# Kernel tuning notes

Hardware: AMD Instinct MI355X
Metric: run time of the kernel (lower is better)

Reference implementation:

```python
import jax, jax.numpy as jnp
import numpy as np

N_NODES = 100000
N_EDGES = 400000
N_GRAPHS = 2500
DIM = 128
F_IN = 78
N_LAYERS = 3
BN_EPS = 1e-5


def setup_inputs() -> dict:
    key = jax.random.key(0)
    ks = jax.random.split(key, 24)
    def lin(k, fi, fo):
        return jax.random.normal(k, (fi, fo), jnp.float32) / np.sqrt(fi)
    inp = {
        "x": jax.random.normal(ks[0], (N_NODES, F_IN), jnp.float32),
        "edge_index": jax.random.randint(ks[1], (2, N_EDGES), 0, N_NODES, jnp.int32),
        "batch": jnp.sort(jax.random.randint(ks[2], (N_NODES,), 0, N_GRAPHS, jnp.int32)),
        "num_graphs": N_GRAPHS,
        "gcn1_W": lin(ks[3], F_IN, DIM), "gcn1_b": jnp.zeros((DIM,), jnp.float32),
        "gcn2_W": lin(ks[4], DIM, DIM), "gcn2_b": jnp.zeros((DIM,), jnp.float32),
        "gin0_w1": lin(ks[5], F_IN, DIM), "gin0_b1": jnp.zeros((DIM,), jnp.float32),
        "gin0_w2": lin(ks[6], DIM, DIM), "gin0_b2": jnp.zeros((DIM,), jnp.float32),
        # layers 1..2 stacked (same 128->128 shapes)
        "gin_w1": jnp.stack([lin(ks[7], DIM, DIM), lin(ks[8], DIM, DIM)]),
        "gin_b1": jnp.zeros((2, DIM), jnp.float32),
        "gin_w2": jnp.stack([lin(ks[9], DIM, DIM), lin(ks[10], DIM, DIM)]),
        "gin_b2": jnp.zeros((2, DIM), jnp.float32),
        "bn_gamma": jnp.ones((N_LAYERS, DIM), jnp.float32),
        "bn_beta": jnp.zeros((N_LAYERS, DIM), jnp.float32),
    }
    return inp


def reference(x, edge_index, batch, num_graphs,
              gcn1_W, gcn1_b, gcn2_W, gcn2_b,
              gin0_w1, gin0_b1, gin0_w2, gin0_b2,
              gin_w1, gin_b1, gin_w2, gin_b2,
              bn_gamma, bn_beta):
    n = x.shape[0]
    src, dst = edge_index[0], edge_index[1]

    def gcn(h, W, b):
        # linear -> symmetric-normalized aggregation with self loops (PyG GCNConv)
        h = h @ W
        loop = jnp.arange(n, dtype=src.dtype)
        s = jnp.concatenate([src, loop])
        d = jnp.concatenate([dst, loop])
        deg = jax.ops.segment_sum(jnp.ones(s.shape[0], h.dtype), d, num_segments=n)
        dis = jax.lax.rsqrt(deg)  # deg >= 1 thanks to self loops
        norm = (dis[s] * dis[d])[:, None]
        return jax.ops.segment_sum(h[s] * norm, d, num_segments=n) + b

    def gin(h, w1, b1, w2, b2):
        # GINConv, eps=0: mlp(x + sum_{j->i} x_j)
        agg = jax.ops.segment_sum(h[src], dst, num_segments=n)
        z = jax.nn.relu((h + agg) @ w1 + b1)
        return z @ w2 + b2

    def bn(h, g, bt):
        mu = h.mean(0)
        var = ((h - mu) ** 2).mean(0)
        return (h - mu) * jax.lax.rsqrt(var + BN_EPS) * g + bt

    g1 = jax.nn.relu(gcn(x, gcn1_W, gcn1_b))
    g2 = jax.nn.relu(gcn(g1, gcn2_W, gcn2_b))
    g2a = g2 + g1
    g2m = g2 * g1

    h = x
    xs = []
    m = jnp.float32(1.0)
    e = jnp.float32(0.0)
    for i in range(N_LAYERS):
        if i == 0:
            h = gin(h, gin0_w1, gin0_b1, gin0_w2, gin0_b2)
        else:
            h = gin(h, gin_w1[i - 1], gin_b1[i - 1], gin_w2[i - 1], gin_b2[i - 1])
        h = bn(jax.nn.relu(h), bn_gamma[i], bn_beta[i])
        m = m * h
        e = e + h
        xs.append(h)

    rep = jnp.concatenate(xs + [m, e, g1, g2, g2a, g2m], axis=-1)  # [N, 9*DIM]
    return jax.ops.segment_max(rep, batch, num_segments=num_graphs)
```

## Files before the change

kernel.cpp:

```cpp
#include <hip/hip_runtime.h>
#include <math.h>

#define DIMC 128
#define FINC 78
#define REPW 1152
#define SCAN_TILE 1024

typedef __attribute__((ext_vector_type(8))) short short8x;
typedef __attribute__((ext_vector_type(4))) float f32x4;

__device__ inline float b2f(unsigned short u) {
    union { unsigned int i; float f; } v; v.i = ((unsigned int)u) << 16; return v.f;
}
__device__ inline unsigned short f2b(float f) {
    union { float f; unsigned int i; } v; v.f = f;
    unsigned int r = (v.i + 0x7FFFu + ((v.i >> 16) & 1u)) >> 16;
    return (unsigned short)r;
}


__global__ void k_fill_int(int* __restrict__ p, int v, int n) {
    int i = blockIdx.x * blockDim.x + threadIdx.x;
    if (i < n) p[i] = v;
}

__global__ void k_fill(float* __restrict__ p, float v, int n) {
    int i = blockIdx.x * blockDim.x + threadIdx.x;
    if (i < n) p[i] = v;
}

__global__ void k_count(const int* __restrict__ dst, int* __restrict__ cnt, int E) {
    int e = blockIdx.x * blockDim.x + threadIdx.x;
    if (e < E) atomicAdd(&cnt[dst[e]], 1);
}

__launch_bounds__(256)
__global__ void k_tilesum(const int* __restrict__ cnt, int* __restrict__ tileSum, int N) {
    __shared__ int red[256];
    int base = blockIdx.x * SCAN_TILE;
    int s = 0;
    for (int i = threadIdx.x; i < SCAN_TILE; i += 256) {
        int idx = base + i;
        if (idx < N) s += cnt[idx];
    }
    red[threadIdx.x] = s;
    __syncthreads();
    for (int d = 128; d > 0; d >>= 1) {
        if (threadIdx.x < d) red[threadIdx.x] += red[threadIdx.x + d];
        __syncthreads();
    }
    if (threadIdx.x == 0) tileSum[blockIdx.x] = red[0];
}

__launch_bounds__(256)
__global__ void k_tilescan(const int* __restrict__ tileSum, int* __restrict__ tileOff,
                           int* __restrict__ rowptr, int T, int N) {
    __shared__ int sh[256];
    int t = threadIdx.x;
    int orig = (t < T) ? tileSum[t] : 0;
    sh[t] = orig;
    __syncthreads();
    for (int d = 1; d < 256; d <<= 1) {
        int v = (t >= d) ? sh[t - d] : 0;
        __syncthreads();
        sh[t] += v;
        __syncthreads();
    }
    if (t < T) tileOff[t] = sh[t] - orig;
    if (t == 255) rowptr[N] = sh[255];
}

__launch_bounds__(256)
__global__ void k_tileemit(const int* __restrict__ cnt, const int* __restrict__ tileOff,
                           int* __restrict__ rowptr, int* __restrict__ cursor,
                           float* __restrict__ dis, int N) {
    __shared__ int sh[256];
    int t = threadIdx.x;
    int base = blockIdx.x * SCAN_TILE;
    int idx0 = base + t * 4;
    int v0 = 0, v1 = 0, v2 = 0, v3 = 0;
    if (idx0 + 3 < N) {
        int4 v = *(const int4*)(cnt + idx0);
        v0 = v.x; v1 = v.y; v2 = v.z; v3 = v.w;
    } else {
        if (idx0 + 0 < N) v0 = cnt[idx0 + 0];
        if (idx0 + 1 < N) v1 = cnt[idx0 + 1];
        if (idx0 + 2 < N) v2 = cnt[idx0 + 2];
        if (idx0 + 3 < N) v3 = cnt[idx0 + 3];
    }
    int s0 = v0, s1 = s0 + v1, s2 = s1 + v2, s3 = s2 + v3;
    sh[t] = s3;
    __syncthreads();
    for (int d = 1; d < 256; d <<= 1) {
        int v = (t >= d) ? sh[t - d] : 0;
        __syncthreads();
        sh[t] += v;
        __syncthreads();
    }
    int gbase = tileOff[blockIdx.x] + ((t == 0) ? 0 : sh[t - 1]);
    int ex[4] = {0, s0, s1, s2};
    int vv[4] = {v0, v1, v2, v3};
#pragma unroll
    for (int j = 0; j < 4; ++j) {
        int idx = idx0 + j;
        if (idx < N) {
            int r = gbase + ex[j];
            rowptr[idx] = r;
            cursor[idx] = r;
            dis[idx] = rsqrtf((float)vv[j] + 1.0f);
        }
    }
}

__global__ void k_scatter(const int* __restrict__ src, const int* __restrict__ dst,
                          int* __restrict__ cursor, int* __restrict__ col, int E) {
    int e = blockIdx.x * blockDim.x + threadIdx.x;
    if (e < E) {
        int pos = atomicAdd(&cursor[dst[e]], 1);
        col[pos] = src[e];
    }
}

__global__ void k_bounds(const int* __restrict__ batch, int* __restrict__ start, int N, int G) {
    int g = blockIdx.x * blockDim.x + threadIdx.x;
    if (g <= G) {
        int lo = 0, hi = N;
        while (lo < hi) { int mid = (lo + hi) >> 1; if (batch[mid] < g) lo = mid + 1; else hi = mid; }
        start[g] = lo;
    }
}


__global__ void k_cvt_w(const float* __restrict__ s0, const float* __restrict__ s1,
                        const float* __restrict__ s2, const float* __restrict__ s3,
                        const float* __restrict__ s4, const float* __restrict__ s5,
                        const float* __restrict__ s6, const float* __restrict__ s7,
                        unsigned short* __restrict__ whi, unsigned short* __restrict__ wlo) {
    int my = blockIdx.y;
    const float* src; int Ksrc, KP; size_t dstoff;
    const size_t o96 = (size_t)128 * 96, o128 = (size_t)128 * 128;
    switch (my) {
        case 0: src = s0; Ksrc = 78;  KP = 96;  dstoff = 0; break;
        case 1: src = s1; Ksrc = 78;  KP = 96;  dstoff = o96; break;
        case 2: src = s2; Ksrc = 128; KP = 128; dstoff = 2 * o96; break;
        case 3: src = s3; Ksrc = 128; KP = 128; dstoff = 2 * o96 + o128; break;
        case 4: src = s4; Ksrc = 128; KP = 128; dstoff = 2 * o96 + 2 * o128; break;
        case 5: src = s5; Ksrc = 128; KP = 128; dstoff = 2 * o96 + 3 * o128; break;
        case 6: src = s6; Ksrc = 128; KP = 128; dstoff = 2 * o96 + 4 * o128; break;
        default: src = s7; Ksrc = 128; KP = 128; dstoff = 2 * o96 + 5 * o128; break;
    }
    int i = blockIdx.x * blockDim.x + threadIdx.x;
    if (i < 128 * KP) {
        int n = i / KP, k = i - n * KP;
        float v = (k < Ksrc) ? src[(size_t)k * DIMC + n] : 0.f;
        unsigned short hi = f2b(v);
        unsigned short lo = f2b(v - b2f(hi));
        whi[dstoff + i] = hi;
        wlo[dstoff + i] = lo;
    }
}


template<int KREAL, int KP>
__launch_bounds__(256)
__global__ void k_gemm_mfma3(const float* __restrict__ A,
                             const unsigned short* __restrict__ Whi,
                             const unsigned short* __restrict__ Wlo,
                             const float* __restrict__ bias,
                             const float* __restrict__ rowScale,
                             const float* __restrict__ inScale,
                             const float* __restrict__ inShift,
                             float* __restrict__ statsOut,
                             float* __restrict__ C, int N, int doRelu) {
    __shared__ unsigned short sAhi[128 * 32];
    __shared__ unsigned short sAlo[128 * 32];
    __shared__ unsigned short sBhi[128 * 32];
    __shared__ unsigned short sBlo[128 * 32];
    __shared__ float sStats[256];
    const int tid = threadIdx.x;
    const int row0 = blockIdx.x * 128;

    const int wave = tid >> 6;
    const int lane = tid & 63;
    const int lm = lane & 15, q = lane >> 4;
    const int wr = (wave >> 1) * 64, wc = (wave & 1) * 64;

    f32x4 acc[4][4];
#pragma unroll
    for (int a = 0; a < 4; ++a)
#pragma unroll
        for (int b = 0; b < 4; ++b) acc[a][b] = (f32x4){0.f, 0.f, 0.f, 0.f};

    for (int k0 = 0; k0 < KP; k0 += 32) {
        if (k0) __syncthreads();
        for (int s = tid; s < 512; s += 256) {
            int r = s >> 2, g = s & 3;
            int gr = row0 + r;
            float v[8];
            int kb = k0 + g * 8;
            if (gr < N) {
                if (KREAL % 8 == 0) {
                    float4 u0 = *(const float4*)(A + (size_t)gr * KREAL + kb);
                    float4 u1 = *(const float4*)(A + (size_t)gr * KREAL + kb + 4);
                    v[0] = u0.x; v[1] = u0.y; v[2] = u0.z; v[3] = u0.w;
                    v[4] = u1.x; v[5] = u1.y; v[6] = u1.z; v[7] = u1.w;
                } else {
#pragma unroll
                    for (int j = 0; j < 8; ++j) {
                        int k = kb + j;
                        v[j] = (k < KREAL) ? A[(size_t)gr * KREAL + k] : 0.f;
                    }
                }
                if (inScale) {
#pragma unroll
                    for (int j = 0; j < 8; ++j) {
                        int k = kb + j;
                        v[j] = fmaf(v[j], inScale[k], inShift[k]);
                    }
                }
            } else {
#pragma unroll
                for (int j = 0; j < 8; ++j) v[j] = 0.f;
            }
            unsigned int hi[4], lo[4];
#pragma unroll
            for (int j = 0; j < 4; ++j) {
                unsigned short h0 = f2b(v[2 * j]), h1 = f2b(v[2 * j + 1]);
                unsigned short l0 = f2b(v[2 * j] - b2f(h0)), l1 = f2b(v[2 * j + 1] - b2f(h1));
                hi[j] = (unsigned int)h0 | ((unsigned int)h1 << 16);
                lo[j] = (unsigned int)l0 | ((unsigned int)l1 << 16);
            }
            size_t addr = ((size_t)g * 128 + ((r + g) & 127)) * 8;
            *(uint4*)(sAhi + addr) = make_uint4(hi[0], hi[1], hi[2], hi[3]);
            *(uint4*)(sAlo + addr) = make_uint4(lo[0], lo[1], lo[2], lo[3]);
        }
        for (int s = tid; s < 512; s += 256) {
            int n = s >> 2, g = s & 3;
            size_t gaddr = (size_t)n * KP + k0 + g * 8;
            size_t addr = ((size_t)g * 128 + ((n + g) & 127)) * 8;
            *(uint4*)(sBhi + addr) = *(const uint4*)(Whi + gaddr);
            *(uint4*)(sBlo + addr) = *(const uint4*)(Wlo + gaddr);
        }
        __syncthreads();

        short8x ah[4], al[4], bh[4], bl[4];
#pragma unroll
        for (int rt = 0; rt < 4; ++rt) {
            int m = wr + rt * 16 + lm;
            size_t addr = ((size_t)q * 128 + ((m + q) & 127)) * 8;
            ah[rt] = *(const short8x*)(sAhi + addr);
            al[rt] = *(const short8x*)(sAlo + addr);
        }
#pragma unroll
        for (int ct = 0; ct < 4; ++ct) {
            int n = wc + ct * 16 + lm;
            size_t addr = ((size_t)q * 128 + ((n + q) & 127)) * 8;
            bh[ct] = *(const short8x*)(sBhi + addr);
            bl[ct] = *(const short8x*)(sBlo + addr);
        }
#pragma unroll
        for (int rt = 0; rt < 4; ++rt)
#pragma unroll
            for (int ct = 0; ct < 4; ++ct) {
                acc[rt][ct] = __builtin_amdgcn_mfma_f32_16x16x32_bf16(ah[rt], bh[ct], acc[rt][ct], 0, 0, 0);
                acc[rt][ct] = __builtin_amdgcn_mfma_f32_16x16x32_bf16(ah[rt], bl[ct], acc[rt][ct], 0, 0, 0);
                acc[rt][ct] = __builtin_amdgcn_mfma_f32_16x16x32_bf16(al[rt], bh[ct], acc[rt][ct], 0, 0, 0);
            }
    }

    float cs[4] = {0.f, 0.f, 0.f, 0.f}, cq[4] = {0.f, 0.f, 0.f, 0.f};
#pragma unroll
    for (int rt = 0; rt < 4; ++rt) {
#pragma unroll
        for (int i = 0; i < 4; ++i) {
            int row = wr + rt * 16 + q * 4 + i;
            int gr = row0 + row;
            if (gr < N) {
                float sc = rowScale ? rowScale[gr] : 1.f;
#pragma unroll
                for (int ct = 0; ct < 4; ++ct) {
                    int colg = wc + ct * 16 + lm;
                    float v = acc[rt][ct][i];
                    if (bias) v += bias[colg];
                    if (doRelu) v = fmaxf(v, 0.f);
                    v *= sc;
                    C[(size_t)gr * DIMC + colg] = v;
                    if (statsOut) { cs[ct] += v; cq[ct] = fmaf(v, v, cq[ct]); }
                }
            }
        }
    }
    if (statsOut) {
        sStats[tid] = 0.f;
        __syncthreads();
#pragma unroll
        for (int ct = 0; ct < 4; ++ct) {
            int colg = wc + ct * 16 + lm;
            atomicAdd(&sStats[colg], cs[ct]);
            atomicAdd(&sStats[128 + colg], cq[ct]);
        }
        __syncthreads();
        atomicAdd(&statsOut[tid], sStats[tid]);
    }
}


__global__ void k_bn_coef(const float* __restrict__ bnsum, const float* __restrict__ gamma,
                          const float* __restrict__ beta, float* __restrict__ coef, float invN) {
    int c = threadIdx.x;
    float mu  = bnsum[c] * invN;
    float var = bnsum[128 + c] * invN - mu * mu;
    float inv = rsqrtf(var + 1e-5f);
    float s = gamma[c] * inv;
    coef[c] = s;
    coef[128 + c] = beta[c] - mu * s;
}


__global__ void k_gather_gcn(const float4* __restrict__ t, const int* __restrict__ rowptr,
                             const int* __restrict__ col, const float* __restrict__ dis,
                             const float4* __restrict__ bias, float4* __restrict__ out, int N) {
    int i = blockIdx.x * blockDim.x + threadIdx.x;
    int node = i >> 5, c4 = i & 31;
    if (node >= N) return;
    int s = rowptr[node], e = rowptr[node + 1];
    float4 acc = t[(size_t)node * 32 + c4];
    for (int k = s; k < e; ++k) {
        float4 v = t[(size_t)col[k] * 32 + c4];
        acc.x += v.x; acc.y += v.y; acc.z += v.z; acc.w += v.w;
    }
    float d = dis[node];
    float4 b = bias[c4];
    float4 o;
    o.x = fmaxf(acc.x * d + b.x, 0.f);
    o.y = fmaxf(acc.y * d + b.y, 0.f);
    o.z = fmaxf(acc.z * d + b.z, 0.f);
    o.w = fmaxf(acc.w * d + b.w, 0.f);
    out[(size_t)node * 32 + c4] = o;
}

__global__ void k_gather_gin(const float4* __restrict__ t, const int* __restrict__ rowptr,
                             const int* __restrict__ col, const float4* __restrict__ bias,
                             float4* __restrict__ out, int N) {
    int i = blockIdx.x * blockDim.x + threadIdx.x;
    int node = i >> 5, c4 = i & 31;
    if (node >= N) return;
    int s = rowptr[node], e = rowptr[node + 1];
    float4 acc = t[(size_t)node * 32 + c4];
    for (int k = s; k < e; ++k) {
        float4 v = t[(size_t)col[k] * 32 + c4];
        acc.x += v.x; acc.y += v.y; acc.z += v.z; acc.w += v.w;
    }
    float4 b = bias[c4];
    float4 o;
    o.x = fmaxf(acc.x + b.x, 0.f);
    o.y = fmaxf(acc.y + b.y, 0.f);
    o.z = fmaxf(acc.z + b.z, 0.f);
    o.w = fmaxf(acc.w + b.w, 0.f);
    out[(size_t)node * 32 + c4] = o;
}


__global__ void k_segmax_gin_all(const float* __restrict__ h0, const float* __restrict__ h1,
                                 const float* __restrict__ h2, const float* __restrict__ coef,
                                 const int* __restrict__ start, float* __restrict__ out) {
    int g = blockIdx.x, c = threadIdx.x;
    float s0 = coef[c],       t0 = coef[128 + c];
    float s1 = coef[256 + c], t1 = coef[384 + c];
    float s2 = coef[512 + c], t2 = coef[640 + c];
    int s = start[g], e = start[g + 1];
    float m0 = -INFINITY, m1 = -INFINITY, m2 = -INFINITY, mm = -INFINITY, me = -INFINITY;
    for (int n = s; n < e; ++n) {
        size_t idx = (size_t)n * DIMC + c;
        float a0 = fmaf(h0[idx], s0, t0);
        float a1 = fmaf(h1[idx], s1, t1);
        float a2 = fmaf(h2[idx], s2, t2);
        m0 = fmaxf(m0, a0); m1 = fmaxf(m1, a1); m2 = fmaxf(m2, a2);
        mm = fmaxf(mm, a0 * a1 * a2);
        me = fmaxf(me, a0 + a1 + a2);
    }
    size_t o = (size_t)g * REPW + c;
    out[o]            = m0;
    out[o + 1 * DIMC] = m1;
    out[o + 2 * DIMC] = m2;
    out[o + 3 * DIMC] = mm;
    out[o + 4 * DIMC] = me;
}

__global__ void k_segmax_gcn(const float* __restrict__ G1, const float* __restrict__ G2,
                             const int* __restrict__ start, float* __restrict__ out) {
    int g = blockIdx.x, c = threadIdx.x;
    int s = start[g], e = start[g + 1];
    float m1 = -INFINITY, m2 = -INFINITY, ma = -INFINITY, mm = -INFINITY;
    for (int n = s; n < e; ++n) {
        float a = G1[(size_t)n * DIMC + c], b = G2[(size_t)n * DIMC + c];
        m1 = fmaxf(m1, a); m2 = fmaxf(m2, b);
        ma = fmaxf(ma, a + b); mm = fmaxf(mm, a * b);
    }
    size_t o = (size_t)g * REPW + c;
    out[o + 5 * DIMC] = m1;
    out[o + 6 * DIMC] = m2;
    out[o + 7 * DIMC] = ma;
    out[o + 8 * DIMC] = mm;
}


extern "C" void kernel_launch(void* const* d_in, const int* in_sizes, int n_in,
                              void* d_out, int out_size, void* d_ws, size_t ws_size,
                              hipStream_t stream) {
    const float* x       = (const float*)d_in[0];
    const int*   ei      = (const int*)d_in[1];
    const int*   batch   = (const int*)d_in[2];
    const float* gcn1_W  = (const float*)d_in[4];
    const float* gcn1_b  = (const float*)d_in[5];
    const float* gcn2_W  = (const float*)d_in[6];
    const float* gcn2_b  = (const float*)d_in[7];
    const float* gin0_w1 = (const float*)d_in[8];
    const float* gin0_b1 = (const float*)d_in[9];
    const float* gin0_w2 = (const float*)d_in[10];
    const float* gin0_b2 = (const float*)d_in[11];
    const float* gin_w1  = (const float*)d_in[12];
    const float* gin_b1  = (const float*)d_in[13];
    const float* gin_w2  = (const float*)d_in[14];
    const float* gin_b2  = (const float*)d_in[15];
    const float* bn_g    = (const float*)d_in[16];
    const float* bn_b    = (const float*)d_in[17];
    float* out = (float*)d_out;

    const int N = in_sizes[0] / FINC;
    const int E = in_sizes[1] / 2;
    const int G = out_size / REPW;
    const int* srcv = ei;
    const int* dstv = ei + E;

    char* ws = (char*)d_ws;
    size_t off = 0;
    auto alloc = [&](size_t bytes) { char* p = ws + off; off += (bytes + 255) & ~(size_t)255; return p; };
    int*   cnt     = (int*)alloc(N * 4);
    int*   rowptr  = (int*)alloc((N + 1) * 4);
    int*   cursor  = (int*)alloc(N * 4);
    int*   col     = (int*)alloc(E * 4);
    float* dis     = (float*)alloc(N * 4);
    float* bnsum   = (float*)alloc(768 * 4);
    float* coef    = (float*)alloc(768 * 4);
    int*   start   = (int*)alloc((G + 1) * 4);
    int*   tileSum = (int*)alloc(256 * 4);
    int*   tileOff = (int*)alloc(256 * 4);
    const size_t wtElems = 2 * (size_t)128 * 96 + 6 * (size_t)128 * 128;
    unsigned short* whi = (unsigned short*)alloc(wtElems * 2);
    unsigned short* wlo = (unsigned short*)alloc(wtElems * 2);
    float* bufT    = (float*)alloc((size_t)N * DIMC * 4);
    float* bufZ    = (float*)alloc((size_t)N * DIMC * 4);
    float* h0      = (float*)alloc((size_t)N * DIMC * 4);
    float* h1      = (float*)alloc((size_t)N * DIMC * 4);
    float* h2      = (float*)alloc((size_t)N * DIMC * 4);
    (void)ws_size; (void)n_in;

    const size_t o96 = (size_t)128 * 96, o128 = (size_t)128 * 128;
    const size_t woff[8] = {0, o96, 2 * o96, 2 * o96 + o128, 2 * o96 + 2 * o128,
                            2 * o96 + 3 * o128, 2 * o96 + 4 * o128, 2 * o96 + 5 * o128};

    const int T = 256;
    auto cdiv = [](long a, long b) { return (int)((a + b - 1) / b); };
    const int gemmGrid = cdiv(N, 128);
    const int gatherGrid = cdiv((long)N * 32, T);
    const int nTiles = cdiv(N, SCAN_TILE);
    const float invN = 1.0f / (float)N;

    k_fill_int<<<cdiv(N, T), T, 0, stream>>>(cnt, 0, N);
    k_count<<<cdiv(E, T), T, 0, stream>>>(dstv, cnt, E);
    k_tilesum<<<nTiles, T, 0, stream>>>(cnt, tileSum, N);
    k_tilescan<<<1, T, 0, stream>>>(tileSum, tileOff, rowptr, nTiles, N);
    k_tileemit<<<nTiles, T, 0, stream>>>(cnt, tileOff, rowptr, cursor, dis, N);
    k_scatter<<<cdiv(E, T), T, 0, stream>>>(srcv, dstv, cursor, col, E);
    k_bounds<<<cdiv(G + 1, T), T, 0, stream>>>(batch, start, N, G);
    k_fill<<<3, T, 0, stream>>>(bnsum, 0.f, 768);
    {
        dim3 g(64, 8);
        k_cvt_w<<<g, T, 0, stream>>>(gcn1_W, gin0_w1, gcn2_W, gin0_w2,
                                     gin_w1, gin_w1 + o128, gin_w2, gin_w2 + o128, whi, wlo);
    }

    k_gemm_mfma3<FINC, 96><<<gemmGrid, T, 0, stream>>>(x, whi + woff[0], wlo + woff[0],
                                                       nullptr, dis, nullptr, nullptr, nullptr, bufT, N, 0);
    k_gather_gcn<<<gatherGrid, T, 0, stream>>>((const float4*)bufT, rowptr, col, dis,
                                               (const float4*)gcn1_b, (float4*)bufZ, N);
    k_gemm_mfma3<DIMC, 128><<<gemmGrid, T, 0, stream>>>(bufZ, whi + woff[2], wlo + woff[2],
                                                        nullptr, dis, nullptr, nullptr, nullptr, bufT, N, 0);
    k_gather_gcn<<<gatherGrid, T, 0, stream>>>((const float4*)bufT, rowptr, col, dis,
                                               (const float4*)gcn2_b, (float4*)h0, N);
    k_segmax_gcn<<<G, DIMC, 0, stream>>>(bufZ, h0, start, out);

    const int w1i[3] = {1, 4, 5};
    const int w2i[3] = {3, 6, 7};
    const float* b1s[3] = {gin0_b1, gin_b1, gin_b1 + DIMC};
    const float* b2s[3] = {gin0_b2, gin_b2, gin_b2 + DIMC};
    float* hs[3] = {h0, h1, h2};

    for (int L = 0; L < 3; ++L) {
        if (L == 0)
            k_gemm_mfma3<FINC, 96><<<gemmGrid, T, 0, stream>>>(x, whi + woff[1], wlo + woff[1],
                                                               nullptr, nullptr, nullptr, nullptr, nullptr,
                                                               bufT, N, 0);
        else
            k_gemm_mfma3<DIMC, 128><<<gemmGrid, T, 0, stream>>>(hs[L - 1], whi + woff[w1i[L]], wlo + woff[w1i[L]],
                                                                nullptr, nullptr,
                                                                coef + (L - 1) * 256, coef + (L - 1) * 256 + 128,
                                                                nullptr, bufT, N, 0);
        k_gather_gin<<<gatherGrid, T, 0, stream>>>((const float4*)bufT, rowptr, col,
                                                   (const float4*)b1s[L], (float4*)bufZ, N);
        k_gemm_mfma3<DIMC, 128><<<gemmGrid, T, 0, stream>>>(bufZ, whi + woff[w2i[L]], wlo + woff[w2i[L]],
                                                            b2s[L], nullptr, nullptr, nullptr,
                                                            bnsum + L * 256, hs[L], N, 1);
        k_bn_coef<<<1, DIMC, 0, stream>>>(bnsum + L * 256, bn_g + L * DIMC, bn_b + L * DIMC,
                                          coef + L * 256, invN);
    }

    k_segmax_gin_all<<<G, DIMC, 0, stream>>>(h0, h1, h2, coef, start, out);
}
```

Measured before the change: 794.1 us.

## Store intermediates as split bf16 hi/lo pairs and fold BN into GIN weights

All node-feature intermediates now live as pairs of bf16 hi/lo arrays instead of fp32. The GEMM loads pre-split operands directly rather than converting fp32 on every tile, and the gathers read and write the hi/lo form eight channels per thread. Batch-norm scale is folded into the next layer's W1 and its shift into a per-column bias applied in the gather, which drops the per-element affine transform in the GEMM prologue. Storage footprint is unchanged, but the gathers and epilogues take on extra pack/unpack work.

```diff
diff --git a/kernel.cpp b/kernel.cpp
--- a/kernel.cpp
+++ b/kernel.cpp
@@ -16,6 +16,26 @@
     union { float f; unsigned int i; } v; v.f = f;
     unsigned int r = (v.i + 0x7FFFu + ((v.i >> 16) & 1u)) >> 16;
     return (unsigned short)r;
+}
+__device__ inline void hl2f8(uint4 h, uint4 l, float* f) {
+    unsigned int hw[4] = {h.x, h.y, h.z, h.w}, lw[4] = {l.x, l.y, l.z, l.w};
+#pragma unroll
+    for (int j = 0; j < 4; ++j) {
+        f[2 * j]     = b2f((unsigned short)(hw[j] & 0xFFFF)) + b2f((unsigned short)(lw[j] & 0xFFFF));
+        f[2 * j + 1] = b2f((unsigned short)(hw[j] >> 16))    + b2f((unsigned short)(lw[j] >> 16));
+    }
+}
+__device__ inline void f82hl(const float* f, uint4& h, uint4& l) {
+    unsigned int hw[4], lw[4];
+#pragma unroll
+    for (int j = 0; j < 4; ++j) {
+        unsigned short h0 = f2b(f[2 * j]), h1 = f2b(f[2 * j + 1]);
+        unsigned short l0 = f2b(f[2 * j] - b2f(h0)), l1 = f2b(f[2 * j + 1] - b2f(h1));
+        hw[j] = (unsigned int)h0 | ((unsigned int)h1 << 16);
+        lw[j] = (unsigned int)l0 | ((unsigned int)l1 << 16);
+    }
+    h = make_uint4(hw[0], hw[1], hw[2], hw[3]);
+    l = make_uint4(lw[0], lw[1], lw[2], lw[3]);
 }
 
 
@@ -131,10 +151,21 @@
 }
 
 
+__global__ void k_cvt_x(const float* __restrict__ x, unsigned short* __restrict__ xhi,
+                        unsigned short* __restrict__ xlo, int N) {
+    int i = blockIdx.x * blockDim.x + threadIdx.x;
+    if (i < N * 96) {
+        int n = i / 96, k = i - n * 96;
+        float v = (k < FINC) ? x[(size_t)n * FINC + k] : 0.f;
+        unsigned short hi = f2b(v);
+        xhi[i] = hi;
+        xlo[i] = f2b(v - b2f(hi));
+    }
+}
+
 __global__ void k_cvt_w(const float* __restrict__ s0, const float* __restrict__ s1,
                         const float* __restrict__ s2, const float* __restrict__ s3,
                         const float* __restrict__ s4, const float* __restrict__ s5,
-                        const float* __restrict__ s6, const float* __restrict__ s7,
                         unsigned short* __restrict__ whi, unsigned short* __restrict__ wlo) {
     int my = blockIdx.y;
     const float* src; int Ksrc, KP; size_t dstoff;
@@ -145,165 +176,50 @@
         case 2: src = s2; Ksrc = 128; KP = 128; dstoff = 2 * o96; break;
         case 3: src = s3; Ksrc = 128; KP = 128; dstoff = 2 * o96 + o128; break;
         case 4: src = s4; Ksrc = 128; KP = 128; dstoff = 2 * o96 + 2 * o128; break;
-        case 5: src = s5; Ksrc = 128; KP = 128; dstoff = 2 * o96 + 3 * o128; break;
-        case 6: src = s6; Ksrc = 128; KP = 128; dstoff = 2 * o96 + 4 * o128; break;
-        default: src = s7; Ksrc = 128; KP = 128; dstoff = 2 * o96 + 5 * o128; break;
+        default: src = s5; Ksrc = 128; KP = 128; dstoff = 2 * o96 + 3 * o128; break;
     }
     int i = blockIdx.x * blockDim.x + threadIdx.x;
     if (i < 128 * KP) {
         int n = i / KP, k = i - n * KP;
         float v = (k < Ksrc) ? src[(size_t)k * DIMC + n] : 0.f;
         unsigned short hi = f2b(v);
-        unsigned short lo = f2b(v - b2f(hi));
+        wlo[dstoff + i] = f2b(v - b2f(hi));
         whi[dstoff + i] = hi;
-        wlo[dstoff + i] = lo;
-    }
-}
-
-
-template<int KREAL, int KP>
+    }
+}
+
+
 __launch_bounds__(256)
-__global__ void k_gemm_mfma3(const float* __restrict__ A,
-                             const unsigned short* __restrict__ Whi,
-                             const unsigned short* __restrict__ Wlo,
-                             const float* __restrict__ bias,
-                             const float* __restrict__ rowScale,
-                             const float* __restrict__ inScale,
-                             const float* __restrict__ inShift,
-                             float* __restrict__ statsOut,
-                             float* __restrict__ C, int N, int doRelu) {
-    __shared__ unsigned short sAhi[128 * 32];
-    __shared__ unsigned short sAlo[128 * 32];
-    __shared__ unsigned short sBhi[128 * 32];
-    __shared__ unsigned short sBlo[128 * 32];
-    __shared__ float sStats[256];
-    const int tid = threadIdx.x;
-    const int row0 = blockIdx.x * 128;
-
-    const int wave = tid >> 6;
-    const int lane = tid & 63;
-    const int lm = lane & 15, q = lane >> 4;
-    const int wr = (wave >> 1) * 64, wc = (wave & 1) * 64;
-
-    f32x4 acc[4][4];
-#pragma unroll
-    for (int a = 0; a < 4; ++a)
-#pragma unroll
-        for (int b = 0; b < 4; ++b) acc[a][b] = (f32x4){0.f, 0.f, 0.f, 0.f};
-
-    for (int k0 = 0; k0 < KP; k0 += 32) {
-        if (k0) __syncthreads();
-        for (int s = tid; s < 512; s += 256) {
-            int r = s >> 2, g = s & 3;
-            int gr = row0 + r;
-            float v[8];
-            int kb = k0 + g * 8;
-            if (gr < N) {
-                if (KREAL % 8 == 0) {
-                    float4 u0 = *(const float4*)(A + (size_t)gr * KREAL + kb);
-                    float4 u1 = *(const float4*)(A + (size_t)gr * KREAL + kb + 4);
-                    v[0] = u0.x; v[1] = u0.y; v[2] = u0.z; v[3] = u0.w;
-                    v[4] = u1.x; v[5] = u1.y; v[6] = u1.z; v[7] = u1.w;
-                } else {
-#pragma unroll
-                    for (int j = 0; j < 8; ++j) {
-                        int k = kb + j;
-                        v[j] = (k < KREAL) ? A[(size_t)gr * KREAL + k] : 0.f;
-                    }
-                }
-                if (inScale) {
-#pragma unroll
-                    for (int j = 0; j < 8; ++j) {
-                        int k = kb + j;
-                        v[j] = fmaf(v[j], inScale[k], inShift[k]);
-                    }
-                }
-            } else {
-#pragma unroll
-                for (int j = 0; j < 8; ++j) v[j] = 0.f;
-            }
-            unsigned int hi[4], lo[4];
-#pragma unroll
-            for (int j = 0; j < 4; ++j) {
-                unsigned short h0 = f2b(v[2 * j]), h1 = f2b(v[2 * j + 1]);
-                unsigned short l0 = f2b(v[2 * j] - b2f(h0)), l1 = f2b(v[2 * j + 1] - b2f(h1));
-                hi[j] = (unsigned int)h0 | ((unsigned int)h1 << 16);
-                lo[j] = (unsigned int)l0 | ((unsigned int)l1 << 16);
-            }
-            size_t addr = ((size_t)g * 128 + ((r + g) & 127)) * 8;
-            *(uint4*)(sAhi + addr) = make_uint4(hi[0], hi[1], hi[2], hi[3]);
-            *(uint4*)(sAlo + addr) = make_uint4(lo[0], lo[1], lo[2], lo[3]);
-        }
-        for (int s = tid; s < 512; s += 256) {
-            int n = s >> 2, g = s & 3;
-            size_t gaddr = (size_t)n * KP + k0 + g * 8;
-            size_t addr = ((size_t)g * 128 + ((n + g) & 127)) * 8;
-            *(uint4*)(sBhi + addr) = *(const uint4*)(Whi + gaddr);
-            *(uint4*)(sBlo + addr) = *(const uint4*)(Wlo + gaddr);
-        }
-        __syncthreads();
-
-        short8x ah[4], al[4], bh[4], bl[4];
-#pragma unroll
-        for (int rt = 0; rt < 4; ++rt) {
-            int m = wr + rt * 16 + lm;
-            size_t addr = ((size_t)q * 128 + ((m + q) & 127)) * 8;
-            ah[rt] = *(const short8x*)(sAhi + addr);
-            al[rt] = *(const short8x*)(sAlo + addr);
-        }
-#pragma unroll
-        for (int ct = 0; ct < 4; ++ct) {
-            int n = wc + ct * 16 + lm;
-            size_t addr = ((size_t)q * 128 + ((n + q) & 127)) * 8;
-            bh[ct] = *(const short8x*)(sBhi + addr);
-            bl[ct] = *(const short8x*)(sBlo + addr);
-        }
-#pragma unroll
-        for (int rt = 0; rt < 4; ++rt)
-#pragma unroll
-            for (int ct = 0; ct < 4; ++ct) {
-                acc[rt][ct] = __builtin_amdgcn_mfma_f32_16x16x32_bf16(ah[rt], bh[ct], acc[rt][ct], 0, 0, 0);
-                acc[rt][ct] = __builtin_amdgcn_mfma_f32_16x16x32_bf16(ah[rt], bl[ct], acc[rt][ct], 0, 0, 0);
-                acc[rt][ct] = __builtin_amdgcn_mfma_f32_16x16x32_bf16(al[rt], bh[ct], acc[rt][ct], 0, 0, 0);
-            }
-    }
-
-    float cs[4] = {0.f, 0.f, 0.f, 0.f}, cq[4] = {0.f, 0.f, 0.f, 0.f};
-#pragma unroll
-    for (int rt = 0; rt < 4; ++rt) {
-#pragma unroll
-        for (int i = 0; i < 4; ++i) {
-            int row = wr + rt * 16 + q * 4 + i;
-            int gr = row0 + row;
-            if (gr < N) {
-                float sc = rowScale ? rowScale[gr] : 1.f;
-#pragma unroll
-                for (int ct = 0; ct < 4; ++ct) {
-                    int colg = wc + ct * 16 + lm;
-                    float v = acc[rt][ct][i];
-                    if (bias) v += bias[colg];
-                    if (doRelu) v = fmaxf(v, 0.f);
-                    v *= sc;
-                    C[(size_t)gr * DIMC + colg] = v;
-                    if (statsOut) { cs[ct] += v; cq[ct] = fmaf(v, v, cq[ct]); }
-                }
-            }
-        }
-    }
-    if (statsOut) {
-        sStats[tid] = 0.f;
-        __syncthreads();
-#pragma unroll
-        for (int ct = 0; ct < 4; ++ct) {
-            int colg = wc + ct * 16 + lm;
-            atomicAdd(&sStats[colg], cs[ct]);
-            atomicAdd(&sStats[128 + colg], cq[ct]);
-        }
-        __syncthreads();
-        atomicAdd(&statsOut[tid], sStats[tid]);
-    }
-}
-
+__global__ void k_bn_w(const float* __restrict__ bnsum, const float* __restrict__ gamma,
+                       const float* __restrict__ beta, const float* __restrict__ w1,
+                       float* __restrict__ coef, unsigned short* __restrict__ whiO,
+                       unsigned short* __restrict__ wloO, float* __restrict__ cbeta, float invN) {
+    __shared__ float sS[128], sT[128], sC[256];
+    int t = threadIdx.x;
+    if (t < 128) {
+        float mu  = bnsum[t] * invN;
+        float var = bnsum[128 + t] * invN - mu * mu;
+        float inv = rsqrtf(var + 1e-5f);
+        float s = gamma[t] * inv;
+        float sh = beta[t] - mu * s;
+        coef[t] = s; coef[128 + t] = sh;
+        sS[t] = s; sT[t] = sh;
+    }
+    __syncthreads();
+    for (int i = t; i < 16384; i += 256) {
+        int n = i >> 7, k = i & 127;
+        float v = w1[(size_t)k * 128 + n] * sS[k];
+        unsigned short hi = f2b(v);
+        whiO[i] = hi;
+        wloO[i] = f2b(v - b2f(hi));
+    }
+    int n = t & 127, half = t >> 7;
+    float acc = 0.f;
+    for (int k = half * 64; k < half * 64 + 64; ++k) acc = fmaf(sT[k], w1[(size_t)k * 128 + n], acc);
+    sC[t] = acc;
+    __syncthreads();
+    if (t < 128) cbeta[t] = sC[t] + sC[t + 128];
+}
 
 __global__ void k_bn_coef(const float* __restrict__ bnsum, const float* __restrict__ gamma,
                           const float* __restrict__ beta, float* __restrict__ coef, float invN) {
@@ -317,53 +233,182 @@
 }
 
 
-__global__ void k_gather_gcn(const float4* __restrict__ t, const int* __restrict__ rowptr,
-                             const int* __restrict__ col, const float* __restrict__ dis,
-                             const float4* __restrict__ bias, float4* __restrict__ out, int N) {
+template<int KP>
+__launch_bounds__(256)
+__global__ void k_gemm_hl(const unsigned short* __restrict__ Ahi,
+                          const unsigned short* __restrict__ Alo,
+                          const unsigned short* __restrict__ Whi,
+                          const unsigned short* __restrict__ Wlo,
+                          const float* __restrict__ bias,
+                          const float* __restrict__ rowScale,
+                          float* __restrict__ statsOut,
+                          unsigned short* __restrict__ Chi,
+                          unsigned short* __restrict__ Clo,
+                          int N, int doRelu) {
+    __shared__ unsigned short sAhi[4096], sAlo[4096], sBhi[4096], sBlo[4096];
+    __shared__ float sStats[256];
+    const int tid = threadIdx.x;
+    const int row0 = blockIdx.x * 128;
+
+    const int wave = tid >> 6;
+    const int lane = tid & 63;
+    const int lm = lane & 15, q = lane >> 4;
+    const int wr = (wave >> 1) * 64, wc = (wave & 1) * 64;
+
+    f32x4 acc[4][4];
+#pragma unroll
+    for (int a = 0; a < 4; ++a)
+#pragma unroll
+        for (int b = 0; b < 4; ++b) acc[a][b] = (f32x4){0.f, 0.f, 0.f, 0.f};
+
+    for (int k0 = 0; k0 < KP; k0 += 32) {
+        if (k0) __syncthreads();
+        for (int s = tid; s < 512; s += 256) {
+            int g = s & 3, r = s >> 2;
+            int gr = row0 + r;
+            size_t la = ((size_t)g * 128 + r) * 8;
+            uint4 vh = make_uint4(0, 0, 0, 0), vl = make_uint4(0, 0, 0, 0);
+            if (gr < N) {
+                size_t ga = (size_t)gr * KP + k0 + g * 8;
+                vh = *(const uint4*)(Ahi + ga);
+                vl = *(const uint4*)(Alo + ga);
+            }
+            *(uint4*)(sAhi + la) = vh;
+            *(uint4*)(sAlo + la) = vl;
+            size_t gb = (size_t)r * KP + k0 + g * 8;
+            *(uint4*)(sBhi + la) = *(const uint4*)(Whi + gb);
+            *(uint4*)(sBlo + la) = *(const uint4*)(Wlo + gb);
+        }
+        __syncthreads();
+
+        short8x ah[4], al[4], bh[4], bl[4];
+#pragma unroll
+        for (int rt = 0; rt < 4; ++rt) {
+            size_t addr = ((size_t)q * 128 + wr + rt * 16 + lm) * 8;
+            ah[rt] = *(const short8x*)(sAhi + addr);
+            al[rt] = *(const short8x*)(sAlo + addr);
+        }
+#pragma unroll
+        for (int ct = 0; ct < 4; ++ct) {
+            size_t addr = ((size_t)q * 128 + wc + ct * 16 + lm) * 8;
+            bh[ct] = *(const short8x*)(sBhi + addr);
+            bl[ct] = *(const short8x*)(sBlo + addr);
+        }
+#pragma unroll
+        for (int rt = 0; rt < 4; ++rt)
+#pragma unroll
+            for (int ct = 0; ct < 4; ++ct) {
+                acc[rt][ct] = __builtin_amdgcn_mfma_f32_16x16x32_bf16(ah[rt], bh[ct], acc[rt][ct], 0, 0, 0);
+                acc[rt][ct] = __builtin_amdgcn_mfma_f32_16x16x32_bf16(ah[rt], bl[ct], acc[rt][ct], 0, 0, 0);
+                acc[rt][ct] = __builtin_amdgcn_mfma_f32_16x16x32_bf16(al[rt], bh[ct], acc[rt][ct], 0, 0, 0);
+            }
+    }
+
+    float cs[4] = {0.f, 0.f, 0.f, 0.f}, cq[4] = {0.f, 0.f, 0.f, 0.f};
+#pragma unroll
+    for (int rt = 0; rt < 4; ++rt) {
+#pragma unroll
+        for (int i = 0; i < 4; ++i) {
+            int row = wr + rt * 16 + q * 4 + i;
+            int gr = row0 + row;
+            if (gr < N) {
+                float sc = rowScale ? rowScale[gr] : 1.f;
+#pragma unroll
+                for (int ct = 0; ct < 4; ++ct) {
+                    int colg = wc + ct * 16 + lm;
+                    float v = acc[rt][ct][i];
+                    if (bias) v += bias[colg];
+                    if (doRelu) v = fmaxf(v, 0.f);
+                    v *= sc;
+                    unsigned short hi = f2b(v);
+                    Chi[(size_t)gr * DIMC + colg] = hi;
+                    Clo[(size_t)gr * DIMC + colg] = f2b(v - b2f(hi));
+                    if (statsOut) { cs[ct] += v; cq[ct] = fmaf(v, v, cq[ct]); }
+                }
+            }
+        }
+    }
+    if (statsOut) {
+        sStats[tid] = 0.f;
+        __syncthreads();
+#pragma unroll
+        for (int ct = 0; ct < 4; ++ct) {
+            int colg = wc + ct * 16 + lm;
+            atomicAdd(&sStats[colg], cs[ct]);
+            atomicAdd(&sStats[128 + colg], cq[ct]);
+        }
+        __syncthreads();
+        atomicAdd(&statsOut[tid], sStats[tid]);
+    }
+}
+
+
+__global__ void k_gather_gcn_hl(const unsigned short* __restrict__ thi, const unsigned short* __restrict__ tlo,
+                                const int* __restrict__ rowptr, const int* __restrict__ col,
+                                const float* __restrict__ dis, const float* __restrict__ bias,
+                                unsigned short* __restrict__ ohi, unsigned short* __restrict__ olo, int N) {
     int i = blockIdx.x * blockDim.x + threadIdx.x;
-    int node = i >> 5, c4 = i & 31;
+    int node = i >> 4, c8 = (i & 15) * 8;
     if (node >= N) return;
     int s = rowptr[node], e = rowptr[node + 1];
-    float4 acc = t[(size_t)node * 32 + c4];
+    float acc[8];
+    hl2f8(*(const uint4*)(thi + (size_t)node * DIMC + c8),
+          *(const uint4*)(tlo + (size_t)node * DIMC + c8), acc);
     for (int k = s; k < e; ++k) {
-        float4 v = t[(size_t)col[k] * 32 + c4];
-        acc.x += v.x; acc.y += v.y; acc.z += v.z; acc.w += v.w;
+        float f[8];
+        size_t a = (size_t)col[k] * DIMC + c8;
+        hl2f8(*(const uint4*)(thi + a), *(const uint4*)(tlo + a), f);
+#pragma unroll
+        for (int j = 0; j < 8; ++j) acc[j] += f[j];
     }
     float d = dis[node];
-    float4 b = bias[c4];
-    float4 o;
-    o.x = fmaxf(acc.x * d + b.x, 0.f);
-    o.y = fmaxf(acc.y * d + b.y, 0.f);
-    o.z = fmaxf(acc.z * d + b.z, 0.f);
-    o.w = fmaxf(acc.w * d + b.w, 0.f);
-    out[(size_t)node * 32 + c4] = o;
-}
-
-__global__ void k_gather_gin(const float4* __restrict__ t, const int* __restrict__ rowptr,
-                             const int* __restrict__ col, const float4* __restrict__ bias,
-                             float4* __restrict__ out, int N) {
+    float o[8];
+#pragma unroll
+    for (int j = 0; j < 8; ++j) o[j] = fmaxf(acc[j] * d + bias[c8 + j], 0.f);
+    uint4 h, l;
+    f82hl(o, h, l);
+    *(uint4*)(ohi + (size_t)node * DIMC + c8) = h;
+    *(uint4*)(olo + (size_t)node * DIMC + c8) = l;
+}
+
+__global__ void k_gather_gin_hl(const unsigned short* __restrict__ thi, const unsigned short* __restrict__ tlo,
+                                const int* __restrict__ rowptr, const int* __restrict__ col,
+                                const float* __restrict__ bias, const float* __restrict__ cbeta,
+                                unsigned short* __restrict__ ohi, unsigned short* __restrict__ olo, int N) {
     int i = blockIdx.x * blockDim.x + threadIdx.x;
-    int node = i >> 5, c4 = i & 31;
+    int node = i >> 4, c8 = (i & 15) * 8;
     if (node >= N) return;
     int s = rowptr[node], e = rowptr[node + 1];
-    float4 acc = t[(size_t)node * 32 + c4];
+    float acc[8];
+    hl2f8(*(const uint4*)(thi + (size_t)node * DIMC + c8),
+          *(const uint4*)(tlo + (size_t)node * DIMC + c8), acc);
     for (int k = s; k < e; ++k) {
-        float4 v = t[(size_t)col[k] * 32 + c4];
-        acc.x += v.x; acc.y += v.y; acc.z += v.z; acc.w += v.w;
-    }
-    float4 b = bias[c4];
-    float4 o;
-    o.x = fmaxf(acc.x + b.x, 0.f);
-    o.y = fmaxf(acc.y + b.y, 0.f);
-    o.z = fmaxf(acc.z + b.z, 0.f);
-    o.w = fmaxf(acc.w + b.w, 0.f);
-    out[(size_t)node * 32 + c4] = o;
-}
-
-
-__global__ void k_segmax_gin_all(const float* __restrict__ h0, const float* __restrict__ h1,
-                                 const float* __restrict__ h2, const float* __restrict__ coef,
-                                 const int* __restrict__ start, float* __restrict__ out) {
+        float f[8];
+        size_t a = (size_t)col[k] * DIMC + c8;
+        hl2f8(*(const uint4*)(thi + a), *(const uint4*)(tlo + a), f);
+#pragma unroll
+        for (int j = 0; j < 8; ++j) acc[j] += f[j];
+    }
+    float deg1 = (float)(e - s + 1);
+    float o[8];
+#pragma unroll
+    for (int j = 0; j < 8; ++j) {
+        float v = acc[j] + bias[c8 + j];
+        if (cbeta) v = fmaf(deg1, cbeta[c8 + j], v);
+        o[j] = fmaxf(v, 0.f);
+    }
+    uint4 h, l;
+    f82hl(o, h, l);
+    *(uint4*)(ohi + (size_t)node * DIMC + c8) = h;
+    *(uint4*)(olo + (size_t)node * DIMC + c8) = l;
+}
+
+
+__global__ void k_segmax_gin_all(const unsigned short* __restrict__ h0h, const unsigned short* __restrict__ h0l,
+                                 const unsigned short* __restrict__ h1h, const unsigned short* __restrict__ h1l,
+                                 const unsigned short* __restrict__ h2h, const unsigned short* __restrict__ h2l,
+                                 const float* __restrict__ coef, const int* __restrict__ start,
+                                 float* __restrict__ out) {
     int g = blockIdx.x, c = threadIdx.x;
     float s0 = coef[c],       t0 = coef[128 + c];
     float s1 = coef[256 + c], t1 = coef[384 + c];
@@ -372,9 +417,9 @@
     float m0 = -INFINITY, m1 = -INFINITY, m2 = -INFINITY, mm = -INFINITY, me = -INFINITY;
     for (int n = s; n < e; ++n) {
         size_t idx = (size_t)n * DIMC + c;
-        float a0 = fmaf(h0[idx], s0, t0);
-        float a1 = fmaf(h1[idx], s1, t1);
-        float a2 = fmaf(h2[idx], s2, t2);
+        float a0 = fmaf(b2f(h0h[idx]) + b2f(h0l[idx]), s0, t0);
+        float a1 = fmaf(b2f(h1h[idx]) + b2f(h1l[idx]), s1, t1);
+        float a2 = fmaf(b2f(h2h[idx]) + b2f(h2l[idx]), s2, t2);
         m0 = fmaxf(m0, a0); m1 = fmaxf(m1, a1); m2 = fmaxf(m2, a2);
         mm = fmaxf(mm, a0 * a1 * a2);
         me = fmaxf(me, a0 + a1 + a2);
@@ -387,13 +432,16 @@
     out[o + 4 * DIMC] = me;
 }
 
-__global__ void k_segmax_gcn(const float* __restrict__ G1, const float* __restrict__ G2,
+__global__ void k_segmax_gcn(const unsigned short* __restrict__ g1h, const unsigned short* __restrict__ g1l,
+                             const unsigned short* __restrict__ g2h, const unsigned short* __restrict__ g2l,
                              const int* __restrict__ start, float* __restrict__ out) {
     int g = blockIdx.x, c = threadIdx.x;
     int s = start[g], e = start[g + 1];
     float m1 = -INFINITY, m2 = -INFINITY, ma = -INFINITY, mm = -INFINITY;
     for (int n = s; n < e; ++n) {
-        float a = G1[(size_t)n * DIMC + c], b = G2[(size_t)n * DIMC + c];
+        size_t idx = (size_t)n * DIMC + c;
+        float a = b2f(g1h[idx]) + b2f(g1l[idx]);
+        float b = b2f(g2h[idx]) + b2f(g2l[idx]);
         m1 = fmaxf(m1, a); m2 = fmaxf(m2, b);
         ma = fmaxf(ma, a + b); mm = fmaxf(mm, a * b);
     }
@@ -433,6 +481,9 @@
     const int* srcv = ei;
     const int* dstv = ei + E;
 
+    auto cdiv = [](long a, long b) { return (int)((a + b - 1) / b); };
+    const int gemmGrid = cdiv(N, 128);
+
     char* ws = (char*)d_ws;
     size_t off = 0;
     auto alloc = [&](size_t bytes) { char* p = ws + off; off += (bytes + 255) & ~(size_t)255; return p; };
@@ -443,27 +494,35 @@
     float* dis     = (float*)alloc(N * 4);
     float* bnsum   = (float*)alloc(768 * 4);
     float* coef    = (float*)alloc(768 * 4);
+    float* cbeta   = (float*)alloc(128 * 4);
     int*   start   = (int*)alloc((G + 1) * 4);
     int*   tileSum = (int*)alloc(256 * 4);
     int*   tileOff = (int*)alloc(256 * 4);
-    const size_t wtElems = 2 * (size_t)128 * 96 + 6 * (size_t)128 * 128;
+    const size_t wtElems = 2 * (size_t)128 * 96 + 4 * (size_t)128 * 128;
     unsigned short* whi = (unsigned short*)alloc(wtElems * 2);
     unsigned short* wlo = (unsigned short*)alloc(wtElems * 2);
-    float* bufT    = (float*)alloc((size_t)N * DIMC * 4);
-    float* bufZ    = (float*)alloc((size_t)N * DIMC * 4);
-    float* h0      = (float*)alloc((size_t)N * DIMC * 4);
-    float* h1      = (float*)alloc((size_t)N * DIMC * 4);
-    float* h2      = (float*)alloc((size_t)N * DIMC * 4);
+    unsigned short* w1shi = (unsigned short*)alloc((size_t)128 * 128 * 2);
+    unsigned short* w1slo = (unsigned short*)alloc((size_t)128 * 128 * 2);
+    const size_t P = (size_t)N * DIMC;
+    unsigned short* tThi = (unsigned short*)alloc(P * 2);
+    unsigned short* tTlo = (unsigned short*)alloc(P * 2);
+    unsigned short* zhi  = (unsigned short*)alloc(P * 2);
+    unsigned short* zlo  = (unsigned short*)alloc(P * 2);
+    unsigned short* h0hi = (unsigned short*)alloc(P * 2);
+    unsigned short* h0lo = (unsigned short*)alloc(P * 2);
+    unsigned short* h1hi = (unsigned short*)alloc(P * 2);
+    unsigned short* h1lo = (unsigned short*)alloc(P * 2);
+    unsigned short* h2hi = (unsigned short*)alloc(P * 2);
+    unsigned short* h2lo = (unsigned short*)alloc(P * 2);
+    unsigned short* xhi = h2hi;
+    unsigned short* xlo = h2lo;
     (void)ws_size; (void)n_in;
 
     const size_t o96 = (size_t)128 * 96, o128 = (size_t)128 * 128;
-    const size_t woff[8] = {0, o96, 2 * o96, 2 * o96 + o128, 2 * o96 + 2 * o128,
-                            2 * o96 + 3 * o128, 2 * o96 + 4 * o128, 2 * o96 + 5 * o128};
+    const size_t woff[6] = {0, o96, 2 * o96, 2 * o96 + o128, 2 * o96 + 2 * o128, 2 * o96 + 3 * o128};
 
     const int T = 256;
-    auto cdiv = [](long a, long b) { return (int)((a + b - 1) / b); };
-    const int gemmGrid = cdiv(N, 128);
-    const int gatherGrid = cdiv((long)N * 32, T);
+    const int gatherGrid = cdiv((long)N * 16, T);
     const int nTiles = cdiv(N, SCAN_TILE);
     const float invN = 1.0f / (float)N;
 
@@ -475,46 +534,49 @@
     k_scatter<<<cdiv(E, T), T, 0, stream>>>(srcv, dstv, cursor, col, E);
     k_bounds<<<cdiv(G + 1, T), T, 0, stream>>>(batch, start, N, G);
     k_fill<<<3, T, 0, stream>>>(bnsum, 0.f, 768);
+    k_cvt_x<<<cdiv((long)N * 96, T), T, 0, stream>>>(x, xhi, xlo, N);
     {
-        dim3 g(64, 8);
+        dim3 g(64, 6);
         k_cvt_w<<<g, T, 0, stream>>>(gcn1_W, gin0_w1, gcn2_W, gin0_w2,
-                                     gin_w1, gin_w1 + o128, gin_w2, gin_w2 + o128, whi, wlo);
-    }
-
-    k_gemm_mfma3<FINC, 96><<<gemmGrid, T, 0, stream>>>(x, whi + woff[0], wlo + woff[0],
-                                                       nullptr, dis, nullptr, nullptr, nullptr, bufT, N, 0);
-    k_gather_gcn<<<gatherGrid, T, 0, stream>>>((const float4*)bufT, rowptr, col, dis,
-                                               (const float4*)gcn1_b, (float4*)bufZ, N);
-    k_gemm_mfma3<DIMC, 128><<<gemmGrid, T, 0, stream>>>(bufZ, whi + woff[2], wlo + woff[2],
-                                                        nullptr, dis, nullptr, nullptr, nullptr, bufT, N, 0);
-    k_gather_gcn<<<gatherGrid, T, 0, stream>>>((const float4*)bufT, rowptr, col, dis,
-                                               (const float4*)gcn2_b, (float4*)h0, N);
-    k_segmax_gcn<<<G, DIMC, 0, stream>>>(bufZ, h0, start, out);
-
-    const int w1i[3] = {1, 4, 5};
-    const int w2i[3] = {3, 6, 7};
-    const float* b1s[3] = {gin0_b1, gin_b1, gin_b1 + DIMC};
-    const float* b2s[3] = {gin0_b2, gin_b2, gin_b2 + DIMC};
-    float* hs[3] = {h0, h1, h2};
-
-    for (int L = 0; L < 3; ++L) {
-        if (L == 0)
-            k_gemm_mfma3<FINC, 96><<<gemmGrid, T, 0, stream>>>(x, whi + woff[1], wlo + woff[1],
-                                                               nullptr, nullptr, nullptr, nullptr, nullptr,
-                                                               bufT, N, 0);
-        else
-            k_gemm_mfma3<DIMC, 128><<<gemmGrid, T, 0, stream>>>(hs[L - 1], whi + woff[w1i[L]], wlo + woff[w1i[L]],
-                                                                nullptr, nullptr,
-                                                                coef + (L - 1) * 256, coef + (L - 1) * 256 + 128,
-                                                                nullptr, bufT, N, 0);
-        k_gather_gin<<<gatherGrid, T, 0, stream>>>((const float4*)bufT, rowptr, col,
-                                                   (const float4*)b1s[L], (float4*)bufZ, N);
-        k_gemm_mfma3<DIMC, 128><<<gemmGrid, T, 0, stream>>>(bufZ, whi + woff[w2i[L]], wlo + woff[w2i[L]],
-                                                            b2s[L], nullptr, nullptr, nullptr,
-                                                            bnsum + L * 256, hs[L], N, 1);
-        k_bn_coef<<<1, DIMC, 0, stream>>>(bnsum + L * 256, bn_g + L * DIMC, bn_b + L * DIMC,
-                                          coef + L * 256, invN);
-    }
-
-    k_segmax_gin_all<<<G, DIMC, 0, stream>>>(h0, h1, h2, coef, start, out);
-}
+                                     gin_w2, gin_w2 + o128, whi, wlo);
+    }
+
+    k_gemm_hl<96><<<gemmGrid, T, 0, stream>>>(xhi, xlo, whi + woff[0], wlo + woff[0],
+                                              nullptr, dis, nullptr, tThi, tTlo, N, 0);
+    k_gather_gcn_hl<<<gatherGrid, T, 0, stream>>>(tThi, tTlo, rowptr, col, dis, gcn1_b,
+                                                  h1hi, h1lo, N);
+    k_gemm_hl<128><<<gemmGrid, T, 0, stream>>>(h1hi, h1lo, whi + woff[2], wlo + woff[2],
+                                               nullptr, dis, nullptr, tThi, tTlo, N, 0);
+    k_gather_gcn_hl<<<gatherGrid, T, 0, stream>>>(tThi, tTlo, rowptr, col, dis, gcn2_b,
+                                                  zhi, zlo, N);
+    k_segmax_gcn<<<G, DIMC, 0, stream>>>(h1hi, h1lo, zhi, zlo, start, out);
+
+    k_gemm_hl<96><<<gemmGrid, T, 0, stream>>>(xhi, xlo, whi + woff[1], wlo + woff[1],
+                                              nullptr, nullptr, nullptr, tThi, tTlo, N, 0);
+    k_gather_gin_hl<<<gatherGrid, T, 0, stream>>>(tThi, tTlo, rowptr, col, gin0_b1, nullptr,
+                                                  zhi, zlo, N);
+    k_gemm_hl<128><<<gemmGrid, T, 0, stream>>>(zhi, zlo, whi + woff[3], wlo + woff[3],
+                                               gin0_b2, nullptr, bnsum, h0hi, h0lo, N, 1);
+
+    const unsigned short* hsrc_hi[2] = {h0hi, h1hi};
+    const unsigned short* hsrc_lo[2] = {h0lo, h1lo};
+    unsigned short* hdst_hi[2] = {h1hi, h2hi};
+    unsigned short* hdst_lo[2] = {h1lo, h2lo};
+    for (int L = 1; L <= 2; ++L) {
+        k_bn_w<<<1, T, 0, stream>>>(bnsum + (L - 1) * 256, bn_g + (L - 1) * DIMC, bn_b + (L - 1) * DIMC,
+                                    gin_w1 + (size_t)(L - 1) * o128, coef + (L - 1) * 256,
+                                    w1shi, w1slo, cbeta, invN);
+        k_gemm_hl<128><<<gemmGrid, T, 0, stream>>>(hsrc_hi[L - 1], hsrc_lo[L - 1], w1shi, w1slo,
+                                                   nullptr, nullptr, nullptr, tThi, tTlo, N, 0);
+        k_gather_gin_hl<<<gatherGrid, T, 0, stream>>>(tThi, tTlo, rowptr, col,
+                                                      gin_b1 + (size_t)(L - 1) * DIMC, cbeta,
+                                                      zhi, zlo, N);
+        k_gemm_hl<128><<<gemmGrid, T, 0, stream>>>(zhi, zlo, whi + woff[3 + L], wlo + woff[3 + L],
+                                                   gin_b2 + (size_t)(L - 1) * DIMC, nullptr,
+                                                   bnsum + L * 256, hdst_hi[L - 1], hdst_lo[L - 1], N, 1);
+    }
+    k_bn_coef<<<1, DIMC, 0, stream>>>(bnsum + 512, bn_g + 2 * DIMC, bn_b + 2 * DIMC, coef + 512, invN);
+
+    k_segmax_gin_all<<<G, DIMC, 0, stream>>>(h0hi, h0lo, h1hi, h1lo, h2hi, h2lo,
+                                             coef, start, out);
+}
```

After: 901.0 us. +13.5%, slower.
